# Kernel tuning notes

Measured on AMD Instinct MI355X. Metric: run time of the kernel, lower is better.

Reference implementation:

```python
import jax, jax.numpy as jnp
import numpy as np

B = 1024      # batch
G = 2000      # num_genes
S = 32        # uniform per-gene feature width (geneid_num[i] == 32 for all i)
M1, M2, M3 = 4096, 2048, 1024  # mul_len1/2/3
H = 64        # hidden width of all small MLPs


def setup_inputs() -> dict:
    key = jax.random.key(0)
    ks = jax.random.split(key, 24)
    n = lambda k, shape, s=0.02: jax.random.normal(k, shape, dtype=jnp.float32) * s
    return {
        # activations
        "x":  jax.random.normal(ks[0], (B, G * S), dtype=jnp.float32),
        "z1": jax.random.normal(ks[1], (B, M1), dtype=jnp.float32),
        "z2": jax.random.normal(ks[2], (B, M2), dtype=jnp.float32),
        "z3": jax.random.normal(ks[3], (B, M3), dtype=jnp.float32),
        # per-gene Linear(S,1) weights, stacked: block-diagonal gene stage
        "Wg": n(ks[4], (G, S)), "bg": n(ks[5], (G,)),
        # fc0: Linear(G, 64); fc1/2/3: Linear(Mi, 64). Layout (in, out).
        "W0": n(ks[6], (G, H)),  "b0": n(ks[7], (H,)),
        "W1": n(ks[8], (M1, H)), "b1": n(ks[9], (H,)),
        "W2": n(ks[10], (M2, H)), "b2": n(ks[11], (H,)),
        "W3": n(ks[12], (M3, H)), "b3": n(ks[13], (H,)),
        # learned fusion weights (init 0.5 in torch)
        "w1": jnp.full((H,), 0.5, jnp.float32),
        "w2": jnp.full((H,), 0.5, jnp.float32),
        "w3": jnp.full((H,), 0.5, jnp.float32),
        # final fc: 64->64->64->1
        "fW1": n(ks[14], (H, H)), "fb1": n(ks[15], (H,)),
        "fW2": n(ks[16], (H, H)), "fb2": n(ks[17], (H,)),
        "fW3": n(ks[18], (H, 1)), "fb3": n(ks[19], (1,)),
    }


def reference(x, z1, z2, z3, Wg, bg, W0, b0, W1, b1, W2, b2, W3, b3,
              w1, w2, w3, fW1, fb1, fW2, fb2, fW3, fb3):
    g, s = Wg.shape
    b = x.shape[0]
    # ragged per-gene Linear(numi,1)+ReLU loop == block-diagonal contraction
    # x: [B, G*S] -> [B, G, S]; gene_outputs: [B, G]
    gene = jax.nn.relu(jnp.einsum('bgs,gs->bg', x.reshape(b, g, s), Wg) + bg)
    h0 = jax.nn.relu(gene @ W0 + b0)                 # fc0(gene_outputs)  [B, 64]
    d1 = jax.nn.relu(z1 @ W1 + b1) * w1 + h0         # fc1(z1)*weights_1 + fc0
    d2 = jax.nn.relu(z2 @ W2 + b2) * w2 + d1         # fc2(z2)*weights_2 + d1
    d3 = jax.nn.relu(z3 @ W3 + b3) * w3 + d2         # fc3(z3)*weights_3 + d2
    h = jax.nn.relu(d3 @ fW1 + fb1)
    h = jax.nn.relu(h @ fW2 + fb2)
    return h @ fW3 + fb3                             # [B, 1]
```

## Files before the change

### kernel.cpp

```cpp
#include <hip/hip_runtime.h>

constexpr int BB = 1024;
constexpr int GG = 2000;
constexpr int SS = 32;
constexpr int K1 = 4096, K2 = 2048, K3 = 1024;

constexpr int BH = BB * 64;

constexpr int Y1P_OFF = 0;
constexpr int Y2P_OFF = 4 * BH;
constexpr int Y3P_OFF = 6 * BH;
constexpr int HP_OFF  = 7 * BH;

constexpr int NCH       = 63;
constexpr int NGENE_BLK = NCH * 32;
constexpr int NGEMM_BLK = 224;
constexpr int KCH       = 1024;

__global__ __launch_bounds__(256, 8) void k1_gene_fc0_zgemm(
    const float* __restrict__ x,  const float* __restrict__ z1,
    const float* __restrict__ z2, const float* __restrict__ z3,
    const float* __restrict__ Wg, const float* __restrict__ bg,
    const float* __restrict__ W0,
    const float* __restrict__ W1, const float* __restrict__ W2,
    const float* __restrict__ W3, float* __restrict__ ws)
{
    __shared__ float lds[6144];
    const int bid = blockIdx.x;
    const int t   = threadIdx.x;

    if (bid >= NGEMM_BLK) {
        const int gid   = bid - NGEMM_BLK;
        const int chunk = gid % NCH;
        const int bgrp  = gid / NCH;
        const int g0    = chunk * 32;
        const int b0    = bgrp * 32;
        const int g     = g0 + (t >> 3);
        const bool gv   = (g < GG);

        float4 wg4 = make_float4(0.f, 0.f, 0.f, 0.f);
        if (gv) wg4 = ((const float4*)Wg)[g0 * 8 + t];
        const float bias = (gv && (t & 7) == 0) ? bg[g] : 0.f;

        const float* xp = gv ? (x + (size_t)b0 * (GG * SS) + g0 * SS + t * 4)
                             : x;
        float* gS = lds;

        for (int ii = 0; ii < 32; ii += 8) {
            float4 xr[8];
            #pragma unroll
            for (int j = 0; j < 8; ++j)
                xr[j] = *(const float4*)(xp + (size_t)(ii + j) * (GG * SS));
            #pragma unroll
            for (int j = 0; j < 8; ++j) {
                float p = (xr[j].x * wg4.x + xr[j].y * wg4.y)
                        + (xr[j].z * wg4.z + xr[j].w * wg4.w);
                p += __shfl_xor(p, 1);
                p += __shfl_xor(p, 2);
                p += __shfl_xor(p, 4);
                if ((t & 7) == 0)
                    gS[(ii + j) * 32 + (t >> 3)] = gv ? fmaxf(p + bias, 0.f) : 0.f;
            }
        }

        const int n = t & 63;
        const int w = t >> 6;
        float w0r[32];
        #pragma unroll
        for (int j = 0; j < 32; ++j) {
            int gj = g0 + j; if (gj >= GG) gj = GG - 1;
            w0r[j] = W0[(size_t)gj * 64 + n];
        }
        __syncthreads();

        float* hp = ws + HP_OFF + (size_t)chunk * BH + (size_t)b0 * 64;
        #pragma unroll
        for (int mi = 0; mi < 8; ++mi) {
            const int m = w * 8 + mi;
            float acc = 0.f;
            #pragma unroll
            for (int jj = 0; jj < 8; ++jj) {
                const float4 g4 = *(const float4*)&gS[m * 32 + jj * 4];
                acc = fmaf(g4.w, w0r[jj * 4 + 3], fmaf(g4.z, w0r[jj * 4 + 2],
                      fmaf(g4.y, w0r[jj * 4 + 1], fmaf(g4.x, w0r[jj * 4 + 0], acc))));
            }
            hp[(size_t)m * 64 + n] = acc;
        }
    } else {
        const int id = bid;
        const float* z; const float* W; int K; int mt; int kslab; float* ys;
        if (id < 128)      { z = z1; W = W1; K = K1; mt = id >> 2; kslab = id & 3;
                             ys = ws + Y1P_OFF + (size_t)kslab * BH; }
        else if (id < 192) { int l = id - 128; z = z2; W = W2; K = K2; mt = l >> 1; kslab = l & 1;
                             ys = ws + Y2P_OFF + (size_t)kslab * BH; }
        else               { int l = id - 192; z = z3; W = W3; K = K3; mt = l; kslab = 0;
                             ys = ws + Y3P_OFF; }

        const int m0    = mt * 32;
        const int kbase = kslab * KCH;
        const int n2    = t & 31;
        const int mq    = t >> 5;
        float* zt = lds;
        float* wt = lds + 2048;

        float2 acc[4];
        #pragma unroll
        for (int j = 0; j < 4; ++j) acc[j] = make_float2(0.f, 0.f);

        for (int kc = 0; kc < KCH / 64; ++kc) {
            const int k0 = kbase + kc * 64;
            {
                const int i0 = t, i1 = t + 256;
                ((float4*)zt)[i0] = *(const float4*)&z[(size_t)(m0 + (i0 >> 4)) * K + k0 + (i0 & 15) * 4];
                ((float4*)zt)[i1] = *(const float4*)&z[(size_t)(m0 + (i1 >> 4)) * K + k0 + (i1 & 15) * 4];
                #pragma unroll
                for (int r = 0; r < 4; ++r) {
                    const int idx = t + r * 256;
                    const int row = idx >> 4;
                    const int c4  = (idx & 15) * 4;
                    *(float4*)&wt[row * 64 + c4] =
                        *(const float4*)&W[(size_t)(k0 + row) * 64 + c4];
                }
            }
            __syncthreads();
            #pragma unroll
            for (int kk = 0; kk < 64; kk += 4) {
                const float2 wv0 = *(const float2*)&wt[(kk + 0) * 64 + n2 * 2];
                const float2 wv1 = *(const float2*)&wt[(kk + 1) * 64 + n2 * 2];
                const float2 wv2 = *(const float2*)&wt[(kk + 2) * 64 + n2 * 2];
                const float2 wv3 = *(const float2*)&wt[(kk + 3) * 64 + n2 * 2];
                #pragma unroll
                for (int j = 0; j < 4; ++j) {
                    const float4 zj = *(const float4*)&zt[(mq * 4 + j) * 64 + kk];
                    acc[j].x = fmaf(zj.x, wv0.x, acc[j].x); acc[j].y = fmaf(zj.x, wv0.y, acc[j].y);
                    acc[j].x = fmaf(zj.y, wv1.x, acc[j].x); acc[j].y = fmaf(zj.y, wv1.y, acc[j].y);
                    acc[j].x = fmaf(zj.z, wv2.x, acc[j].x); acc[j].y = fmaf(zj.z, wv2.y, acc[j].y);
                    acc[j].x = fmaf(zj.w, wv3.x, acc[j].x); acc[j].y = fmaf(zj.w, wv3.y, acc[j].y);
                }
            }
            __syncthreads();
        }
        #pragma unroll
        for (int j = 0; j < 4; ++j)
            *(float2*)&ys[(size_t)(m0 + mq * 4 + j) * 64 + n2 * 2] = acc[j];
    }
}

__global__ __launch_bounds__(256, 4) void k2_combine_mlp(
    const float* __restrict__ ws,
    const float* __restrict__ b0v,
    const float* __restrict__ b1v, const float* __restrict__ b2v,
    const float* __restrict__ b3v,
    const float* __restrict__ w1v, const float* __restrict__ w2v,
    const float* __restrict__ w3v,
    const float* __restrict__ fW1, const float* __restrict__ fb1,
    const float* __restrict__ fW2, const float* __restrict__ fb2,
    const float* __restrict__ fW3, const float* __restrict__ fb3,
    float* __restrict__ out)
{
    const float* Y1p = ws + Y1P_OFF;
    const float* Y2p = ws + Y2P_OFF;
    const float* Y3p = ws + Y3P_OFF;

    const int t   = threadIdx.x;
    const int n   = t & 63;
    const int w   = t >> 6;
    const int row = blockIdx.x * 4 + w;
    const int rn  = row * 64 + n;

    float h = 0.f;
    const float* hp = ws + HP_OFF + rn;
    #pragma unroll 9
    for (int c = 0; c < NCH; ++c) h += hp[(size_t)c * BH];
    const float h0 = fmaxf(h + b0v[n], 0.f);

    const float y1 = Y1p[rn] + Y1p[BH + rn] + Y1p[2 * BH + rn] + Y1p[3 * BH + rn];
    float d = fmaf(fmaxf(y1 + b1v[n], 0.f), w1v[n], h0);
    const float y2 = Y2p[rn] + Y2p[BH + rn];
    d = fmaf(fmaxf(y2 + b2v[n], 0.f), w2v[n], d);
    const float y3 = Y3p[rn];
    d = fmaf(fmaxf(y3 + b3v[n], 0.f), w3v[n], d);

    __shared__ float sd[4][64];
    __shared__ float sh[4][64];
    sd[w][n] = d;
    __syncthreads();
    float a1 = fb1[n];
    #pragma unroll 8
    for (int j = 0; j < 64; ++j) a1 = fmaf(sd[w][j], fW1[j * 64 + n], a1);
    a1 = fmaxf(a1, 0.f);
    sh[w][n] = a1;
    __syncthreads();
    float a2 = fb2[n];
    #pragma unroll 8
    for (int j = 0; j < 64; ++j) a2 = fmaf(sh[w][j], fW2[j * 64 + n], a2);
    a2 = fmaxf(a2, 0.f);

    float v = a2 * fW3[n];
    #pragma unroll
    for (int o = 32; o > 0; o >>= 1) v += __shfl_xor(v, o);
    if (n == 0) out[row] = v + fb3[0];
}

extern "C" void kernel_launch(void* const* d_in, const int* in_sizes, int n_in,
                              void* d_out, int out_size, void* d_ws, size_t ws_size,
                              hipStream_t stream)
{
    const float* x   = (const float*)d_in[0];
    const float* z1  = (const float*)d_in[1];
    const float* z2  = (const float*)d_in[2];
    const float* z3  = (const float*)d_in[3];
    const float* Wg  = (const float*)d_in[4];
    const float* bg  = (const float*)d_in[5];
    const float* W0  = (const float*)d_in[6];
    const float* b0v = (const float*)d_in[7];
    const float* W1  = (const float*)d_in[8];
    const float* b1v = (const float*)d_in[9];
    const float* W2  = (const float*)d_in[10];
    const float* b2v = (const float*)d_in[11];
    const float* W3  = (const float*)d_in[12];
    const float* b3v = (const float*)d_in[13];
    const float* w1v = (const float*)d_in[14];
    const float* w2v = (const float*)d_in[15];
    const float* w3v = (const float*)d_in[16];
    const float* fW1 = (const float*)d_in[17];
    const float* fb1 = (const float*)d_in[18];
    const float* fW2 = (const float*)d_in[19];
    const float* fb2 = (const float*)d_in[20];
    const float* fW3 = (const float*)d_in[21];
    const float* fb3 = (const float*)d_in[22];

    float* ws  = (float*)d_ws;
    float* out = (float*)d_out;

    k1_gene_fc0_zgemm<<<dim3(NGEMM_BLK + NGENE_BLK), dim3(256), 0, stream>>>(
        x, z1, z2, z3, Wg, bg, W0, W1, W2, W3, ws);

    k2_combine_mlp<<<dim3(BB / 4), dim3(256), 0, stream>>>(
        ws, b0v, b1v, b2v, b3v, w1v, w2v, w3v,
        fW1, fb1, fW2, fb2, fW3, fb3, out);
}
```

Baseline: 426.0 us.

## Halve gene-stage batch rows per block, LDS reduction, padded smaller GEMM tiles

The gene stage now handles 16 batch rows per block instead of 32, doubling the gene block count. The shuffle-based 8-lane reduction is replaced by writing partial products to LDS and reducing them in a separate pass. The fc0 W0 weights are streamed from global memory rather than held in 32 registers. The z-GEMM path uses 32-wide K chunks with padded LDS strides (36/68) to avoid bank conflicts, and shared memory shrinks overall to raise occupancy, at the cost of extra syncs and more loop iterations.

```diff
diff --git a/kernel.cpp b/kernel.cpp
--- a/kernel.cpp
+++ b/kernel.cpp
@@ -13,7 +13,8 @@
 constexpr int HP_OFF  = 7 * BH;
 
 constexpr int NCH       = 63;
-constexpr int NGENE_BLK = NCH * 32;
+constexpr int RPB       = 16;
+constexpr int NGENE_BLK = NCH * (BB / RPB);
 constexpr int NGEMM_BLK = 224;
 constexpr int KCH       = 1024;
 
@@ -25,7 +26,7 @@
     const float* __restrict__ W1, const float* __restrict__ W2,
     const float* __restrict__ W3, float* __restrict__ ws)
 {
-    __shared__ float lds[6144];
+    __shared__ float lds[4608];
     const int bid = blockIdx.x;
     const int t   = threadIdx.x;
 
@@ -34,19 +35,23 @@
         const int chunk = gid % NCH;
         const int bgrp  = gid / NCH;
         const int g0    = chunk * 32;
-        const int b0    = bgrp * 32;
-        const int g     = g0 + (t >> 3);
+        const int b0    = bgrp * RPB;
+        const int gene  = t >> 3;
+        const int sub   = t & 7;
+        const int g     = g0 + gene;
         const bool gv   = (g < GG);
 
         float4 wg4 = make_float4(0.f, 0.f, 0.f, 0.f);
-        if (gv) wg4 = ((const float4*)Wg)[g0 * 8 + t];
-        const float bias = (gv && (t & 7) == 0) ? bg[g] : 0.f;
-
-        const float* xp = gv ? (x + (size_t)b0 * (GG * SS) + g0 * SS + t * 4)
+        if (gv) wg4 = ((const float4*)Wg)[g * 8 + sub];
+
+        const float* xp = gv ? (x + (size_t)b0 * (GG * SS) + (size_t)g * SS + sub * 4)
                              : x;
-        float* gS = lds;
-
-        for (int ii = 0; ii < 32; ii += 8) {
+
+        float* part = lds;
+        float* gS   = lds + 4096;
+
+        #pragma unroll
+        for (int ii = 0; ii < RPB; ii += 8) {
             float4 xr[8];
             #pragma unroll
             for (int j = 0; j < 8; ++j)
@@ -55,37 +60,40 @@
             for (int j = 0; j < 8; ++j) {
                 float p = (xr[j].x * wg4.x + xr[j].y * wg4.y)
                         + (xr[j].z * wg4.z + xr[j].w * wg4.w);
-                p += __shfl_xor(p, 1);
-                p += __shfl_xor(p, 2);
-                p += __shfl_xor(p, 4);
-                if ((t & 7) == 0)
-                    gS[(ii + j) * 32 + (t >> 3)] = gv ? fmaxf(p + bias, 0.f) : 0.f;
+                part[(ii + j) * 256 + t] = p;
             }
         }
+        __syncthreads();
+
+        #pragma unroll
+        for (int p = t; p < RPB * 32; p += 256) {
+            const float4 a = *(const float4*)&part[p * 8];
+            const float4 b = *(const float4*)&part[p * 8 + 4];
+            float s = ((a.x + a.y) + (a.z + a.w)) + ((b.x + b.y) + (b.z + b.w));
+            const int gg = g0 + (p & 31);
+            const float bias = (gg < GG) ? bg[gg] : 0.f;
+            gS[p] = fmaxf(s + bias, 0.f);
+        }
+        __syncthreads();
 
         const int n = t & 63;
         const int w = t >> 6;
-        float w0r[32];
-        #pragma unroll
+        float acc0 = 0.f, acc1 = 0.f, acc2 = 0.f, acc3 = 0.f;
+        const float* gSw = gS + (w * 4) * 32;
+        #pragma unroll 8
         for (int j = 0; j < 32; ++j) {
             int gj = g0 + j; if (gj >= GG) gj = GG - 1;
-            w0r[j] = W0[(size_t)gj * 64 + n];
-        }
-        __syncthreads();
-
+            const float w0v = W0[(size_t)gj * 64 + n];
+            acc0 = fmaf(gSw[j],      w0v, acc0);
+            acc1 = fmaf(gSw[32 + j], w0v, acc1);
+            acc2 = fmaf(gSw[64 + j], w0v, acc2);
+            acc3 = fmaf(gSw[96 + j], w0v, acc3);
+        }
         float* hp = ws + HP_OFF + (size_t)chunk * BH + (size_t)b0 * 64;
-        #pragma unroll
-        for (int mi = 0; mi < 8; ++mi) {
-            const int m = w * 8 + mi;
-            float acc = 0.f;
-            #pragma unroll
-            for (int jj = 0; jj < 8; ++jj) {
-                const float4 g4 = *(const float4*)&gS[m * 32 + jj * 4];
-                acc = fmaf(g4.w, w0r[jj * 4 + 3], fmaf(g4.z, w0r[jj * 4 + 2],
-                      fmaf(g4.y, w0r[jj * 4 + 1], fmaf(g4.x, w0r[jj * 4 + 0], acc))));
-            }
-            hp[(size_t)m * 64 + n] = acc;
-        }
+        hp[(size_t)(w * 4 + 0) * 64 + n] = acc0;
+        hp[(size_t)(w * 4 + 1) * 64 + n] = acc1;
+        hp[(size_t)(w * 4 + 2) * 64 + n] = acc2;
+        hp[(size_t)(w * 4 + 3) * 64 + n] = acc3;
     } else {
         const int id = bid;
         const float* z; const float* W; int K; int mt; int kslab; float* ys;
@@ -101,37 +109,35 @@
         const int n2    = t & 31;
         const int mq    = t >> 5;
         float* zt = lds;
-        float* wt = lds + 2048;
+        float* wt = lds + 32 * 36;
 
         float2 acc[4];
         #pragma unroll
         for (int j = 0; j < 4; ++j) acc[j] = make_float2(0.f, 0.f);
 
-        for (int kc = 0; kc < KCH / 64; ++kc) {
-            const int k0 = kbase + kc * 64;
-            {
-                const int i0 = t, i1 = t + 256;
-                ((float4*)zt)[i0] = *(const float4*)&z[(size_t)(m0 + (i0 >> 4)) * K + k0 + (i0 & 15) * 4];
-                ((float4*)zt)[i1] = *(const float4*)&z[(size_t)(m0 + (i1 >> 4)) * K + k0 + (i1 & 15) * 4];
-                #pragma unroll
-                for (int r = 0; r < 4; ++r) {
-                    const int idx = t + r * 256;
-                    const int row = idx >> 4;
-                    const int c4  = (idx & 15) * 4;
-                    *(float4*)&wt[row * 64 + c4] =
-                        *(const float4*)&W[(size_t)(k0 + row) * 64 + c4];
-                }
+        const int zr = t >> 3, zc = (t & 7) * 4;
+        for (int kc = 0; kc < KCH / 32; ++kc) {
+            const int k0 = kbase + kc * 32;
+            *(float4*)&zt[zr * 36 + zc] =
+                *(const float4*)&z[(size_t)(m0 + zr) * K + k0 + zc];
+            #pragma unroll
+            for (int r = 0; r < 2; ++r) {
+                const int idx = t + r * 256;
+                const int row = idx >> 4;
+                const int c4  = (idx & 15) * 4;
+                *(float4*)&wt[row * 68 + c4] =
+                    *(const float4*)&W[(size_t)(k0 + row) * 64 + c4];
             }
             __syncthreads();
             #pragma unroll
-            for (int kk = 0; kk < 64; kk += 4) {
-                const float2 wv0 = *(const float2*)&wt[(kk + 0) * 64 + n2 * 2];
-                const float2 wv1 = *(const float2*)&wt[(kk + 1) * 64 + n2 * 2];
-                const float2 wv2 = *(const float2*)&wt[(kk + 2) * 64 + n2 * 2];
-                const float2 wv3 = *(const float2*)&wt[(kk + 3) * 64 + n2 * 2];
+            for (int kk = 0; kk < 32; kk += 4) {
+                const float2 wv0 = *(const float2*)&wt[(kk + 0) * 68 + n2 * 2];
+                const float2 wv1 = *(const float2*)&wt[(kk + 1) * 68 + n2 * 2];
+                const float2 wv2 = *(const float2*)&wt[(kk + 2) * 68 + n2 * 2];
+                const float2 wv3 = *(const float2*)&wt[(kk + 3) * 68 + n2 * 2];
                 #pragma unroll
                 for (int j = 0; j < 4; ++j) {
-                    const float4 zj = *(const float4*)&zt[(mq * 4 + j) * 64 + kk];
+                    const float4 zj = *(const float4*)&zt[(mq * 4 + j) * 36 + kk];
                     acc[j].x = fmaf(zj.x, wv0.x, acc[j].x); acc[j].y = fmaf(zj.x, wv0.y, acc[j].y);
                     acc[j].x = fmaf(zj.y, wv1.x, acc[j].x); acc[j].y = fmaf(zj.y, wv1.y, acc[j].y);
                     acc[j].x = fmaf(zj.z, wv2.x, acc[j].x); acc[j].y = fmaf(zj.z, wv2.y, acc[j].y);
```

Measured after the change: 436.6 us. 2.5% more time.
